# Performance work log

Measured on AMD Instinct MI355X. Metric: run time of the kernel, lower is better.

Reference implementation:

```python
import jax, jax.numpy as jnp
import numpy as np

T, S, W, D, C, K = 16, 16, 10, 512, 64, 512  # tasks, shots, ways, z_dim, n_concept, triplets/group


def setup_inputs() -> dict:
    key = jax.random.key(0)
    ks = jax.random.split(key, 12)
    sc = 0.02
    inp = {
        "input_data": jax.random.normal(ks[0], (T, S, W, D), dtype=jnp.float32),
        "triplet_idx": jax.random.randint(ks[1], (T, W, 3, K), 0, S * W, dtype=jnp.int64),
        # proj_inner: Linear(3D -> 2D), ReLU, Linear(2D -> D)
        "W1": jax.random.normal(ks[2], (3 * D, 2 * D), dtype=jnp.float32) * sc,
        "b1": jnp.zeros((2 * D,), dtype=jnp.float32),
        "W2": jax.random.normal(ks[3], (2 * D, D), dtype=jnp.float32) * sc,
        "b2": jnp.zeros((D,), dtype=jnp.float32),
        # proj_outer: Linear(D -> 2D), ReLU, Linear(2D -> D)
        "W3": jax.random.normal(ks[4], (D, 2 * D), dtype=jnp.float32) * sc,
        "b3": jnp.zeros((2 * D,), dtype=jnp.float32),
        "W4": jax.random.normal(ks[5], (2 * D, D), dtype=jnp.float32) * sc,
        "b4": jnp.zeros((D,), dtype=jnp.float32),
        # cls: Linear(D -> C)
        "Wc": jax.random.normal(ks[6], (D, C), dtype=jnp.float32) * sc,
        "bc": jnp.zeros((C,), dtype=jnp.float32),
    }
    return inp


def reference(input_data, triplet_idx, W1, b1, W2, b2, W3, b3, W4, b4, Wc, bc):
    t, s, w, d = input_data.shape
    x = input_data.reshape(t, s * w, d)                     # [T, N, D], N = shot*way
    # gather triplet embeddings: [T, W, 3, K, D]
    emb = x[jnp.arange(t)[:, None, None, None], triplet_idx]
    # permute([1,0,2]).reshape(-1, 3*dim): [T, W, K, 3*D]
    trip = jnp.swapaxes(emb, 2, 3).reshape(t, w, -1, 3 * d)
    # proj_inner MLP then sum over triplets
    h = jax.nn.relu(trip @ W1 + b1) @ W2 + b2               # [T, W, K, D]
    g = jnp.sum(h, axis=2)                                  # [T, W, D]
    # proj_outer MLP -> cls -> softmax
    o = jax.nn.relu(g @ W3 + b3) @ W4 + b4                  # [T, W, D]
    score = o @ Wc + bc                                     # [T, W, C]
    return jax.nn.softmax(score, axis=-1)
```

## Files before the change

kernel.cpp:

```cpp
#include <hip/hip_runtime.h>
#include <hip/hip_bf16.h>

#define T_  16
#define W_  10
#define D_  512
#define SW_ 160
#define N1_ 1024
#define KT_ 512

typedef __bf16 bf16x8 __attribute__((ext_vector_type(8)));
typedef _Float16 f16x8 __attribute__((ext_vector_type(8)));
typedef float  f32x4  __attribute__((ext_vector_type(4)));
typedef float  f32x2  __attribute__((ext_vector_type(2)));

__device__ __forceinline__ void async16(const void* g, void* l) {
  __builtin_amdgcn_global_load_lds(
      (__attribute__((address_space(1))) void*)(g),
      (__attribute__((address_space(3))) void*)(l), 16, 0, 0);
}

__device__ __forceinline__ f32x2 unpk(unsigned v) {
  return (f32x2){__uint_as_float(v << 16), __uint_as_float(v & 0xffff0000u)};
}
__device__ __forceinline__ f32x2 max0(f32x2 v) {
  return (f32x2){fmaxf(v.x, 0.f), fmaxf(v.y, 0.f)};
}

__global__ __launch_bounds__(256) void prep_all(
    const float* __restrict__ x_in, const float* __restrict__ W1,
    const float* __restrict__ W2, const float* __restrict__ W3,
    const float* __restrict__ W4, const float* __restrict__ Wc,
    const float* __restrict__ b2, const float* __restrict__ b3,
    const float* __restrict__ b4, const float* __restrict__ bc,
    __hip_bfloat16* __restrict__ xbf, __hip_bfloat16* __restrict__ w1t,
    _Float16* __restrict__ w2b, _Float16* __restrict__ w3t,
    _Float16* __restrict__ w4b, _Float16* __restrict__ wct,
    float* __restrict__ b23, float* __restrict__ bc4)
{
  __shared__ float tile[32 * 33];
  const int b = blockIdx.x, tid = threadIdx.x;

  auto cast4h = [&](const float* src, _Float16* dst, int base) {
    int i = (base + tid) << 2;
    float4 v = *(const float4*)(src + i);
    __align__(8) _Float16 o4[4] = {(_Float16)v.x, (_Float16)v.y,
                                   (_Float16)v.z, (_Float16)v.w};
    *(uint2*)(dst + i) = *(const uint2*)o4;
  };
  auto tr32h = [&](const float* src, _Float16* dst, int R, int C, int rt, int ct) {
    int r0 = rt << 5, c0 = ct << 5;
    int c = tid & 31, rr = tid >> 5;
#pragma unroll
    for (int i = 0; i < 4; ++i) {
      int r = rr + i * 8;
      tile[r * 33 + c] = src[(size_t)(r0 + r) * C + c0 + c];
    }
    __syncthreads();
#pragma unroll
    for (int i = 0; i < 4; ++i) {
      int r = rr + i * 8;
      dst[(size_t)(c0 + r) * R + r0 + c] = (_Float16)tile[c * 33 + r];
    }
  };

  if (b < 1280) {
    int i = (b * 256 + tid) << 2;
    float4 v = *(const float4*)(x_in + i);
    __align__(8) __hip_bfloat16 o4[4];
    o4[0] = __float2bfloat16(v.x); o4[1] = __float2bfloat16(v.y);
    o4[2] = __float2bfloat16(v.z); o4[3] = __float2bfloat16(v.w);
    *(uint2*)(xbf + i) = *(const uint2*)o4;
  } else if (b < 2816) {
    int q = b - 1280;
    int r0 = (q >> 5) << 5, c0 = (q & 31) << 5;
    int c = tid & 31, rr = tid >> 5;
#pragma unroll
    for (int i = 0; i < 4; ++i) {
      int r = rr + i * 8;
      tile[r * 33 + c] = W1[(size_t)(r0 + r) * 1024 + c0 + c];
    }
    __syncthreads();
#pragma unroll
    for (int i = 0; i < 4; ++i) {
      int r = rr + i * 8;
      w1t[(size_t)(c0 + r) * 1536 + r0 + c] = __float2bfloat16(tile[c * 33 + r]);
    }
  } else if (b < 3328) {
    cast4h(W2, w2b, (b - 2816) * 256);
  } else if (b < 3840) {
    int q = b - 3328; tr32h(W3, w3t, 512, 1024, q >> 5, q & 31);
  } else if (b < 4352) {
    cast4h(W4, w4b, (b - 3840) * 256);
  } else if (b < 4384) {
    int q = b - 4352; tr32h(Wc, wct, 512, 64, q >> 1, q & 1);
  } else if (b < 4388) {
    int c = (b - 4384) * 256 + tid;
    float s = 0.f;
#pragma unroll 32
    for (int j = 0; j < 512; ++j) s += b2[j] * W3[(size_t)j * 1024 + c];
    b23[c] = 512.f * s + b3[c];
  } else {
    if (tid < 64) {
      float s = 0.f;
#pragma unroll 32
      for (int j = 0; j < 512; ++j) s += b4[j] * Wc[(size_t)j * 64 + tid];
      bc4[tid] = s + bc[tid];
    }
  }
}

__global__ __launch_bounds__(256) void group_wgemm(
    const __hip_bfloat16* __restrict__ xbf,
    const __hip_bfloat16* __restrict__ w1t,
    const int* __restrict__ tidx,
    const float* __restrict__ b1,
    _Float16* __restrict__ Hsb,
    const _Float16* __restrict__ w3t,
    const _Float16* __restrict__ w2b,
    const _Float16* __restrict__ wct,
    const _Float16* __restrict__ w4b,
    _Float16* __restrict__ w23t,
    _Float16* __restrict__ w4ct)
{
  __shared__ __align__(16) char smem[47360];
  const int bx = blockIdx.x;
  const int tid = threadIdx.x;
  const int ln = tid & 63, wv = tid >> 6;
  const int col16 = ln & 15, quad = ln >> 4;

  if (bx >= 512) {
    const int b = bx - 512;
    const _Float16 *A, *Bt;
    _Float16* out;
    int m0, n0;
    if (b < 256) { A = w3t; Bt = w2b; out = w23t; m0 = (b >> 4) << 6; n0 = (b & 15) << 6; }
    else         { A = wct; Bt = w4b; out = w4ct; m0 = 0;             n0 = (b - 256) << 6; }
    char* Abuf = smem;
    char* Bbuf = smem + 16384;

    f32x4 acc[4];
#pragma unroll
    for (int a = 0; a < 4; ++a) acc[a] = (f32x4){0.f, 0.f, 0.f, 0.f};

#pragma unroll 1
    for (int kk = 0; kk < 512; kk += 128) {
      __syncthreads();
#pragma unroll
      for (int p = 0; p < 4; ++p) {
        int i = p * 256 + tid, r = i >> 4, q = i & 15;
        async16(A + (size_t)(m0 + r) * 512 + kk + ((q ^ (r & 7)) << 3), Abuf + (i << 4));
      }
#pragma unroll
      for (int p = 0; p < 4; ++p) {
        int i = p * 256 + tid, r = i >> 4, q = i & 15;
        async16(Bt + (size_t)(n0 + r) * 512 + kk + ((q ^ (r & 7)) << 3), Bbuf + (i << 4));
      }
      __syncthreads();

#pragma unroll
      for (int ks = 0; ks < 4; ++ks) {
        const int qq = (ks << 2) + quad;
        const int rn = (wv << 4) + col16;
        f16x8 bfm = *(const f16x8*)(Bbuf + rn * 256 + ((qq ^ (rn & 7)) << 4));
#pragma unroll
        for (int a = 0; a < 4; ++a) {
          int rm = (a << 4) + col16;
          f16x8 af = *(const f16x8*)(Abuf + rm * 256 + ((qq ^ (rm & 7)) << 4));
          acc[a] = __builtin_amdgcn_mfma_f32_16x16x32_f16(af, bfm, acc[a], 0, 0, 0);
        }
      }
    }

    const int n = n0 + (wv << 4) + col16;
#pragma unroll
    for (int a = 0; a < 4; ++a)
#pragma unroll
      for (int r = 0; r < 4; ++r) {
        size_t row = m0 + (a << 4) + (quad << 2) + r;
        out[row * 1024 + n] = (_Float16)acc[a][r];
      }
    return;
  }

  char* Abuf  = smem;
  char* Bbuf  = smem + 20480;
  char* Ptile = smem;
  int*  idxA  = (int*)(smem + 34560);
  int*  idxB  = (int*)(smem + 40704);
  float* red  = (float*)(smem + 46848);

  const int t   = bx >> 5;
  const int nt  = bx & 31;
  const int n0  = nt << 5;

  const int wr = wv >> 1, wc = wv & 1;

  const __hip_bfloat16* xt = xbf + (size_t)t * (SW_ * D_);

  int aoff[5], lofA[5];
#pragma unroll
  for (int s = 0; s < 5; ++s) {
    int i = s * 256 + tid, r = i >> 3, q = i & 7;
    aoff[s] = r * 512 + ((q ^ (r & 7)) << 3);
    lofA[s] = i << 4;
  }
  int boff[3], lofB[3];
#pragma unroll
  for (int s = 0; s < 3; ++s) {
    int i = s * 256 + tid, r = i >> 3, q = i & 7;
    int nc = r & 31, j = r >> 5;
    boff[s] = (n0 + nc) * 1536 + j * 512 + ((q ^ (r & 7)) << 3);
    lofB[s] = i << 4;
  }

  f32x4 acc[5][3];
#pragma unroll
  for (int a = 0; a < 5; ++a)
#pragma unroll
    for (int b = 0; b < 3; ++b)
      acc[a][b] = (f32x4){0.f, 0.f, 0.f, 0.f};

#pragma unroll 1
  for (int kk = 0; kk < 512; kk += 64) {
    __syncthreads();
#pragma unroll
    for (int s = 0; s < 5; ++s) async16(xt + aoff[s] + kk, Abuf + lofA[s]);
#pragma unroll
    for (int s = 0; s < 3; ++s) async16(w1t + boff[s] + kk, Bbuf + lofB[s]);
    __syncthreads();

#pragma unroll
    for (int ks = 0; ks < 2; ++ks) {
      const int qq = (ks << 2) + quad;
      bf16x8 af[5], bfr[3];
#pragma unroll
      for (int a = 0; a < 5; ++a) {
        int rm = wr * 80 + a * 16 + col16;
        af[a] = *(const bf16x8*)(Abuf + rm * 128 + ((qq ^ (rm & 7)) << 4));
      }
#pragma unroll
      for (int b = 0; b < 3; ++b) {
        int rn = wc * 48 + b * 16 + col16;
        bfr[b] = *(const bf16x8*)(Bbuf + rn * 128 + ((qq ^ (rn & 7)) << 4));
      }
#pragma unroll
      for (int a = 0; a < 5; ++a)
#pragma unroll
        for (int b = 0; b < 3; ++b)
          acc[a][b] = __builtin_amdgcn_mfma_f32_16x16x32_bf16(af[a], bfr[b], acc[a][b], 0, 0, 0);
    }
  }

  __syncthreads();

#pragma unroll
  for (int a = 0; a < 5; ++a)
#pragma unroll
    for (int b = 0; b < 3; ++b) {
      int c = wc * 48 + b * 16 + col16;
      int j = c >> 5, nc = c & 31;
      int mb = wr * 80 + a * 16 + quad * 4;
#pragma unroll
      for (int r = 0; r < 4; ++r)
        *(__hip_bfloat16*)(Ptile + (j * 160 + mb + r) * 72 + nc * 2) =
            __float2bfloat16(acc[a][b][r]);
    }

  const int nq = tid & 7;
  const int kq = tid >> 3;
  const float4 bias4 = *(const float4*)(b1 + n0 + (nq << 2));
  const f32x2 bl = (f32x2){bias4.x, bias4.y};
  const f32x2 bh = (f32x2){bias4.z, bias4.w};
  const char* Pt0 = Ptile + (nq << 3);
  const char* Pt1 = Pt0 + 11520;
  const char* Pt2 = Pt0 + 23040;

  const int* tsrc = tidx + (size_t)t * 10 * 1536;
  int4 ra = make_int4(0, 0, 0, 0), rb = make_int4(0, 0, 0, 0);
  auto sst = [&](int* dst, int4 a, int4 b) {
    *(int4*)(dst + (tid << 2)) = make_int4(a.x * 72, a.y * 72, a.z * 72, a.w * 72);
    if (tid < 128)
      *(int4*)(dst + 1024 + (tid << 2)) = make_int4(b.x * 72, b.y * 72, b.z * 72, b.w * 72);
  };

  ra = *(const int4*)(tsrc + (tid << 2));
  if (tid < 128) rb = *(const int4*)(tsrc + 1024 + (tid << 2));
  sst(idxA, ra, rb);
  int* cur = idxA;
  int* nxt = idxB;

#pragma unroll 1
  for (int w = 0; w < 10; ++w) {
    __syncthreads();
    if (w < 9) {
      const int* s2 = tsrc + (w + 1) * 1536;
      ra = *(const int4*)(s2 + (tid << 2));
      if (tid < 128) rb = *(const int4*)(s2 + 1024 + (tid << 2));
    }

    f32x2 z2 = (f32x2){0.f, 0.f};
    f32x2 acc01 = z2, acc23 = z2;
#pragma unroll
    for (int u = 0; u < 4; ++u) {
      const int kb = (kq << 4) + (u << 2);
      int4 i0 = *(const int4*)(cur + kb);
      int4 i1 = *(const int4*)(cur + 512 + kb);
      int4 i2 = *(const int4*)(cur + 1024 + kb);
#define STEP(IA, IB, IC)                                                  \
      {                                                                   \
        uint2 p0 = *(const uint2*)(Pt0 + (IA));                           \
        uint2 p1 = *(const uint2*)(Pt1 + (IB));                           \
        uint2 p2 = *(const uint2*)(Pt2 + (IC));                           \
        f32x2 s0 = (unpk(p0.x) + unpk(p1.x)) + (unpk(p2.x) + bl);         \
        f32x2 s1 = (unpk(p0.y) + unpk(p1.y)) + (unpk(p2.y) + bh);         \
        acc01 += max0(s0);                                                \
        acc23 += max0(s1);                                                \
      }
      STEP(i0.x, i1.x, i2.x)
      STEP(i0.y, i1.y, i2.y)
      STEP(i0.z, i1.z, i2.z)
      STEP(i0.w, i1.w, i2.w)
#undef STEP
    }

    if (w < 9) sst(nxt, ra, rb);

    f32x4 a4 = (f32x4){acc01.x, acc01.y, acc23.x, acc23.y};
#pragma unroll
    for (int off = 8; off <= 32; off <<= 1) {
      a4.x += __shfl_xor(a4.x, off);
      a4.y += __shfl_xor(a4.y, off);
      a4.z += __shfl_xor(a4.z, off);
      a4.w += __shfl_xor(a4.w, off);
    }
    if ((ln >> 3) == 0)
      *(f32x4*)(red + wv * 32 + (nq << 2)) = a4;
    __syncthreads();
    if (tid < 32) {
      float s = red[tid] + red[32 + tid] + red[64 + tid] + red[96 + tid];
      Hsb[(size_t)(t * 10 + w) * N1_ + n0 + tid] = (_Float16)s;
    }
    int* tmp = cur; cur = nxt; nxt = tmp;
  }
}

__global__ __launch_bounds__(256) void mid_gemm(
    const _Float16* __restrict__ A,
    const _Float16* __restrict__ Bt,
    const float* __restrict__ bias,
    _Float16* __restrict__ out)
{
  __shared__ __align__(16) char Abuf[40960];
  __shared__ __align__(16) char Bbuf[32768];
  const int tid = threadIdx.x;
  const int n0 = blockIdx.x << 6;
  const int m0 = blockIdx.y * 80;
  const int ln = tid & 63, wv = tid >> 6;
  const int col16 = ln & 15, quad = ln >> 4;

  f32x4 acc[5];
#pragma unroll
  for (int a = 0; a < 5; ++a) acc[a] = (f32x4){0.f, 0.f, 0.f, 0.f};

#pragma unroll 1
  for (int kk = 0; kk < 1024; kk += 256) {
    __syncthreads();
#pragma unroll
    for (int p = 0; p < 10; ++p) {
      int i = p * 256 + tid, r = i >> 5, q = i & 31;
      async16(A + (size_t)(m0 + r) * 1024 + kk + ((q ^ (r & 7)) << 3), Abuf + (i << 4));
    }
#pragma unroll
    for (int p = 0; p < 8; ++p) {
      int i = p * 256 + tid, r = i >> 5, q = i & 31;
      async16(Bt + (size_t)(n0 + r) * 1024 + kk + ((q ^ (r & 7)) << 3), Bbuf + (i << 4));
    }
    __syncthreads();

#pragma unroll
    for (int ks = 0; ks < 8; ++ks) {
      const int qq = (ks << 2) + quad;
      const int rn = (wv << 4) + col16;
      f16x8 bfm = *(const f16x8*)(Bbuf + rn * 512 + ((qq ^ (rn & 7)) << 4));
#pragma unroll
      for (int a = 0; a < 5; ++a) {
        int rm = (a << 4) + col16;
        f16x8 af = *(const f16x8*)(Abuf + rm * 512 + ((qq ^ (rm & 7)) << 4));
        acc[a] = __builtin_amdgcn_mfma_f32_16x16x32_f16(af, bfm, acc[a], 0, 0, 0);
      }
    }
  }

  const int n = n0 + (wv << 4) + col16;
  const float bb = bias[n];
#pragma unroll
  for (int a = 0; a < 5; ++a)
#pragma unroll
    for (int r = 0; r < 4; ++r) {
      float v = fmaxf(acc[a][r] + bb, 0.f);
      out[(size_t)(m0 + (a << 4) + (quad << 2) + r) * 1024 + n] = (_Float16)v;
    }
}

__global__ __launch_bounds__(256) void head_gemm2(
    const _Float16* __restrict__ A,
    const _Float16* __restrict__ Bt,
    const float* __restrict__ bc4,
    float* __restrict__ out)
{
  __shared__ __align__(16) char Abuf[40960];
  __shared__ __align__(16) char Bbuf[32768];
  __shared__ float sc[80 * 64];
  __shared__ float rs[80];
  const int tid = threadIdx.x;
  const int m0 = blockIdx.x * 80;
  const int ln = tid & 63, wv = tid >> 6;
  const int col16 = ln & 15, quad = ln >> 4;

  f32x4 acc[5];
#pragma unroll
  for (int a = 0; a < 5; ++a) acc[a] = (f32x4){0.f, 0.f, 0.f, 0.f};

#pragma unroll 1
  for (int kk = 0; kk < 1024; kk += 256) {
    __syncthreads();
#pragma unroll
    for (int p = 0; p < 10; ++p) {
      int i = p * 256 + tid, r = i >> 5, q = i & 31;
      async16(A + (size_t)(m0 + r) * 1024 + kk + ((q ^ (r & 7)) << 3), Abuf + (i << 4));
    }
#pragma unroll
    for (int p = 0; p < 8; ++p) {
      int i = p * 256 + tid, r = i >> 5, q = i & 31;
      async16(Bt + (size_t)r * 1024 + kk + ((q ^ (r & 7)) << 3), Bbuf + (i << 4));
    }
    __syncthreads();

#pragma unroll
    for (int ks = 0; ks < 8; ++ks) {
      const int qq = (ks << 2) + quad;
      const int rn = (wv << 4) + col16;
      f16x8 bfm = *(const f16x8*)(Bbuf + rn * 512 + ((qq ^ (rn & 7)) << 4));
#pragma unroll
      for (int a = 0; a < 5; ++a) {
        int rm = (a << 4) + col16;
        f16x8 af = *(const f16x8*)(Abuf + rm * 512 + ((qq ^ (rm & 7)) << 4));
        acc[a] = __builtin_amdgcn_mfma_f32_16x16x32_f16(af, bfm, acc[a], 0, 0, 0);
      }
    }
  }

  const int n = (wv << 4) + col16;
  const float bb = bc4[n];
#pragma unroll
  for (int a = 0; a < 5; ++a)
#pragma unroll
    for (int r = 0; r < 4; ++r)
      sc[((a << 4) + (quad << 2) + r) * 64 + n] = acc[a][r] + bb;
  __syncthreads();

  if (tid < 80) {
    float m = -1e30f;
    for (int c = 0; c < 64; ++c) m = fmaxf(m, sc[tid * 64 + c]);
    float s = 0.f;
    for (int c = 0; c < 64; ++c) {
      float e = expf(sc[tid * 64 + c] - m);
      sc[tid * 64 + c] = e;
      s += e;
    }
    rs[tid] = 1.f / s;
  }
  __syncthreads();
#pragma unroll
  for (int p = 0; p < 20; ++p) {
    int f = p * 256 + tid, r = f >> 6, c = f & 63;
    out[(size_t)(m0 + r) * 64 + c] = sc[f] * rs[r];
  }
}

extern "C" void kernel_launch(void* const* d_in, const int* in_sizes, int n_in,
                              void* d_out, int out_size, void* d_ws, size_t ws_size,
                              hipStream_t stream) {
  const float* x_in = (const float*)d_in[0];
  const int*   tidx = (const int*)d_in[1];
  const float* W1 = (const float*)d_in[2];
  const float* b1 = (const float*)d_in[3];
  const float* W2 = (const float*)d_in[4];
  const float* b2 = (const float*)d_in[5];
  const float* W3 = (const float*)d_in[6];
  const float* b3 = (const float*)d_in[7];
  const float* W4 = (const float*)d_in[8];
  const float* b4 = (const float*)d_in[9];
  const float* Wc = (const float*)d_in[10];
  const float* bc = (const float*)d_in[11];
  float* out = (float*)d_out;
  (void)in_sizes; (void)n_in; (void)out_size; (void)ws_size;

  char* ws = (char*)d_ws;
  __hip_bfloat16* xbf  = (__hip_bfloat16*)(ws + 0);
  __hip_bfloat16* w1t  = (__hip_bfloat16*)(ws + 2621440);
  _Float16*       w2b  = (_Float16*)      (ws + 5767168);
  _Float16*       w3t  = (_Float16*)      (ws + 6815744);
  _Float16*       w4b  = (_Float16*)      (ws + 7864320);
  _Float16*       wct  = (_Float16*)      (ws + 8912896);
  float*          b23  = (float*)         (ws + 8978432);
  float*          bc4  = (float*)         (ws + 8982528);
  _Float16*       Hsb  = (_Float16*)      (ws + 8982784);
  _Float16*       w23t = (_Float16*)      (ws + 9310464);
  _Float16*       w4ct = (_Float16*)      (ws + 11407616);
  _Float16*       ub   = (_Float16*)      (ws + 11538688);

  prep_all<<<4389, 256, 0, stream>>>(x_in, W1, W2, W3, W4, Wc, b2, b3, b4, bc,
                                     xbf, w1t, w2b, w3t, w4b, wct, b23, bc4);

  group_wgemm<<<784, 256, 0, stream>>>(xbf, w1t, tidx, b1, Hsb,
                                       w3t, w2b, wct, w4b, w23t, w4ct);

  mid_gemm<<<dim3(16, 2), 256, 0, stream>>>(Hsb, w23t, b23, ub);

  head_gemm2<<<2, 256, 0, stream>>>(ub, w4ct, bc4, out);
}
```

Baseline: 156.3 us.

## Split triplet gather into separate kernel and use packed fp16 ReLU accumulation

The projection GEMM kernel now adds the bias, stores its partial tile as fp16 to a global buffer and exits. A new gather kernel, launched over (way-pair, n-tile, task), reloads that tile into LDS and performs the triplet gather, ReLU and sum. This spreads the previously serial 10-way gather loop across many more blocks. The inner loop switches to packed fp16 adds with v_pk_max_f16, replacing fp32 unpacking. This adds global round-trip traffic and a launch, and reduces the accumulation precision.

```diff
diff --git a/kernel.cpp b/kernel.cpp
--- a/kernel.cpp
+++ b/kernel.cpp
@@ -10,8 +10,8 @@
 
 typedef __bf16 bf16x8 __attribute__((ext_vector_type(8)));
 typedef _Float16 f16x8 __attribute__((ext_vector_type(8)));
+typedef _Float16 h2v  __attribute__((ext_vector_type(2)));
 typedef float  f32x4  __attribute__((ext_vector_type(4)));
-typedef float  f32x2  __attribute__((ext_vector_type(2)));
 
 __device__ __forceinline__ void async16(const void* g, void* l) {
   __builtin_amdgcn_global_load_lds(
@@ -19,11 +19,11 @@
       (__attribute__((address_space(3))) void*)(l), 16, 0, 0);
 }
 
-__device__ __forceinline__ f32x2 unpk(unsigned v) {
-  return (f32x2){__uint_as_float(v << 16), __uint_as_float(v & 0xffff0000u)};
-}
-__device__ __forceinline__ f32x2 max0(f32x2 v) {
-  return (f32x2){fmaxf(v.x, 0.f), fmaxf(v.y, 0.f)};
+__device__ __forceinline__ h2v bc2(unsigned u) { return __builtin_bit_cast(h2v, u); }
+__device__ __forceinline__ h2v relu2(h2v a) {
+  h2v r;
+  asm("v_pk_max_f16 %0, %1, 0" : "=v"(r) : "v"(a));
+  return r;
 }
 
 __global__ __launch_bounds__(256) void prep_all(
@@ -109,12 +109,11 @@
   }
 }
 
-__global__ __launch_bounds__(256) void group_wgemm(
+__global__ __launch_bounds__(256) void pgemm_wgemm(
     const __hip_bfloat16* __restrict__ xbf,
     const __hip_bfloat16* __restrict__ w1t,
-    const int* __restrict__ tidx,
     const float* __restrict__ b1,
-    _Float16* __restrict__ Hsb,
+    char* __restrict__ pbuf,
     const _Float16* __restrict__ w3t,
     const _Float16* __restrict__ w2b,
     const _Float16* __restrict__ wct,
@@ -122,7 +121,7 @@
     _Float16* __restrict__ w23t,
     _Float16* __restrict__ w4ct)
 {
-  __shared__ __align__(16) char smem[47360];
+  __shared__ __align__(16) char smem[34560];
   const int bx = blockIdx.x;
   const int tid = threadIdx.x;
   const int ln = tid & 63, wv = tid >> 6;
@@ -185,9 +184,6 @@
   char* Abuf  = smem;
   char* Bbuf  = smem + 20480;
   char* Ptile = smem;
-  int*  idxA  = (int*)(smem + 34560);
-  int*  idxB  = (int*)(smem + 40704);
-  float* red  = (float*)(smem + 46848);
 
   const int t   = bx >> 5;
   const int nt  = bx & 31;
@@ -254,67 +250,91 @@
   __syncthreads();
 
 #pragma unroll
-  for (int a = 0; a < 5; ++a)
-#pragma unroll
-    for (int b = 0; b < 3; ++b) {
-      int c = wc * 48 + b * 16 + col16;
-      int j = c >> 5, nc = c & 31;
+  for (int b = 0; b < 3; ++b) {
+    int c = wc * 48 + b * 16 + col16;
+    int j = c >> 5, nc = c & 31;
+    float bv = (j == 2) ? b1[n0 + nc] : 0.f;
+#pragma unroll
+    for (int a = 0; a < 5; ++a) {
       int mb = wr * 80 + a * 16 + quad * 4;
 #pragma unroll
       for (int r = 0; r < 4; ++r)
-        *(__hip_bfloat16*)(Ptile + (j * 160 + mb + r) * 72 + nc * 2) =
-            __float2bfloat16(acc[a][b][r]);
-    }
+        *(_Float16*)(Ptile + (j * 160 + mb + r) * 72 + nc * 2) =
+            (_Float16)(acc[a][b][r] + bv);
+    }
+  }
+  __syncthreads();
+
+  char* gP = pbuf + (size_t)bx * 34560;
+#pragma unroll
+  for (int p = 0; p < 9; ++p) {
+    int i = p * 256 + tid;
+    if (i < 2160)
+      *(uint4*)(gP + (size_t)i * 16) = *(const uint4*)(Ptile + i * 16);
+  }
+}
+
+__global__ __launch_bounds__(256) void gather_kernel(
+    const char* __restrict__ pbuf,
+    const int* __restrict__ tidx,
+    _Float16* __restrict__ Hsb)
+{
+  __shared__ __align__(16) char P[34560];
+  __shared__ int idx[2][1536];
+  __shared__ float red[2][128];
+  const int tid = threadIdx.x;
+  const int wp  = blockIdx.x;
+  const int win = blockIdx.y;
+  const int t   = blockIdx.z;
+  const int ln = tid & 63, wv = tid >> 6;
+
+  const char* ps = pbuf + (size_t)(t * 32 + win) * 34560;
+#pragma unroll
+  for (int p = 0; p < 9; ++p) {
+    int i = p * 256 + tid;
+    if (i < 2160) async16(ps + (size_t)i * 16, P + i * 16);
+  }
+
+  const int* isrc = tidx + (size_t)(t * 10 + wp * 2) * 1536;
+#pragma unroll
+  for (int v = 0; v < 2; ++v) {
+    const int* s = isrc + v * 1536;
+    int4 ra = *(const int4*)(s + (tid << 2));
+    *(int4*)(&idx[v][tid << 2]) =
+        make_int4(ra.x * 72, ra.y * 72, ra.z * 72, ra.w * 72);
+    if (tid < 128) {
+      int4 rb = *(const int4*)(s + 1024 + (tid << 2));
+      *(int4*)(&idx[v][1024 + (tid << 2)]) =
+          make_int4(rb.x * 72, rb.y * 72, rb.z * 72, rb.w * 72);
+    }
+  }
+  __syncthreads();
 
   const int nq = tid & 7;
   const int kq = tid >> 3;
-  const float4 bias4 = *(const float4*)(b1 + n0 + (nq << 2));
-  const f32x2 bl = (f32x2){bias4.x, bias4.y};
-  const f32x2 bh = (f32x2){bias4.z, bias4.w};
-  const char* Pt0 = Ptile + (nq << 3);
+  const char* Pt0 = P + (nq << 3);
   const char* Pt1 = Pt0 + 11520;
   const char* Pt2 = Pt0 + 23040;
 
-  const int* tsrc = tidx + (size_t)t * 10 * 1536;
-  int4 ra = make_int4(0, 0, 0, 0), rb = make_int4(0, 0, 0, 0);
-  auto sst = [&](int* dst, int4 a, int4 b) {
-    *(int4*)(dst + (tid << 2)) = make_int4(a.x * 72, a.y * 72, a.z * 72, a.w * 72);
-    if (tid < 128)
-      *(int4*)(dst + 1024 + (tid << 2)) = make_int4(b.x * 72, b.y * 72, b.z * 72, b.w * 72);
-  };
-
-  ra = *(const int4*)(tsrc + (tid << 2));
-  if (tid < 128) rb = *(const int4*)(tsrc + 1024 + (tid << 2));
-  sst(idxA, ra, rb);
-  int* cur = idxA;
-  int* nxt = idxB;
-
-#pragma unroll 1
-  for (int w = 0; w < 10; ++w) {
-    __syncthreads();
-    if (w < 9) {
-      const int* s2 = tsrc + (w + 1) * 1536;
-      ra = *(const int4*)(s2 + (tid << 2));
-      if (tid < 128) rb = *(const int4*)(s2 + 1024 + (tid << 2));
-    }
-
-    f32x2 z2 = (f32x2){0.f, 0.f};
-    f32x2 acc01 = z2, acc23 = z2;
+#pragma unroll
+  for (int v = 0; v < 2; ++v) {
+    const int* cid = idx[v];
+    h2v acc01 = (h2v)0, acc23 = (h2v)0;
 #pragma unroll
     for (int u = 0; u < 4; ++u) {
       const int kb = (kq << 4) + (u << 2);
-      int4 i0 = *(const int4*)(cur + kb);
-      int4 i1 = *(const int4*)(cur + 512 + kb);
-      int4 i2 = *(const int4*)(cur + 1024 + kb);
+      int4 i0 = *(const int4*)(cid + kb);
+      int4 i1 = *(const int4*)(cid + 512 + kb);
+      int4 i2 = *(const int4*)(cid + 1024 + kb);
 #define STEP(IA, IB, IC)                                                  \
       {                                                                   \
         uint2 p0 = *(const uint2*)(Pt0 + (IA));                           \
         uint2 p1 = *(const uint2*)(Pt1 + (IB));                           \
         uint2 p2 = *(const uint2*)(Pt2 + (IC));                           \
-        f32x2 s0 = (unpk(p0.x) + unpk(p1.x)) + (unpk(p2.x) + bl);         \
-        f32x2 s1 = (unpk(p0.y) + unpk(p1.y)) + (unpk(p2.y) + bh);         \
-        acc01 += max0(s0);                                                \
-        acc23 += max0(s1);                                                \
+        h2v sx = bc2(p0.x) + bc2(p1.x) + bc2(p2.x);                       \
+        h2v sy = bc2(p0.y) + bc2(p1.y) + bc2(p2.y);                       \
+        acc01 += relu2(sx);                                               \
+        acc23 += relu2(sy);                                               \
       }
       STEP(i0.x, i1.x, i2.x)
       STEP(i0.y, i1.y, i2.y)
@@ -323,9 +343,8 @@
 #undef STEP
     }
 
-    if (w < 9) sst(nxt, ra, rb);
-
-    f32x4 a4 = (f32x4){acc01.x, acc01.y, acc23.x, acc23.y};
+    f32x4 a4 = (f32x4){(float)acc01.x, (float)acc01.y,
+                       (float)acc23.x, (float)acc23.y};
 #pragma unroll
     for (int off = 8; off <= 32; off <<= 1) {
       a4.x += __shfl_xor(a4.x, off);
@@ -334,13 +353,13 @@
       a4.w += __shfl_xor(a4.w, off);
     }
     if ((ln >> 3) == 0)
-      *(f32x4*)(red + wv * 32 + (nq << 2)) = a4;
-    __syncthreads();
-    if (tid < 32) {
-      float s = red[tid] + red[32 + tid] + red[64 + tid] + red[96 + tid];
-      Hsb[(size_t)(t * 10 + w) * N1_ + n0 + tid] = (_Float16)s;
-    }
-    int* tmp = cur; cur = nxt; nxt = tmp;
+      *(f32x4*)(&red[v][wv * 32 + (nq << 2)]) = a4;
+  }
+  __syncthreads();
+  if (tid < 64) {
+    int v = tid >> 5, c = tid & 31;
+    float s = red[v][c] + red[v][32 + c] + red[v][64 + c] + red[v][96 + c];
+    Hsb[(size_t)(t * 10 + wp * 2 + v) * N1_ + (win << 5) + c] = (_Float16)s;
   }
 }
 
@@ -508,14 +527,17 @@
   _Float16*       Hsb  = (_Float16*)      (ws + 8982784);
   _Float16*       w23t = (_Float16*)      (ws + 9310464);
   _Float16*       w4ct = (_Float16*)      (ws + 11407616);
+  char*           pbuf = ws + 11538688;
   _Float16*       ub   = (_Float16*)      (ws + 11538688);
 
   prep_all<<<4389, 256, 0, stream>>>(x_in, W1, W2, W3, W4, Wc, b2, b3, b4, bc,
                                      xbf, w1t, w2b, w3t, w4b, wct, b23, bc4);
 
-  group_wgemm<<<784, 256, 0, stream>>>(xbf, w1t, tidx, b1, Hsb,
+  pgemm_wgemm<<<784, 256, 0, stream>>>(xbf, w1t, b1, pbuf,
                                        w3t, w2b, wct, w4b, w23t, w4ct);
 
+  gather_kernel<<<dim3(5, 32, 16), 256, 0, stream>>>(pbuf, tidx, Hsb);
+
   mid_gemm<<<dim3(16, 2), 256, 0, stream>>>(Hsb, w23t, b23, ub);
 
   head_gemm2<<<2, 256, 0, stream>>>(ub, w4ct, bc4, out);
```

Measured after the change: 160.7 us. 1.03x slower.
